# Optimization experiments

Hardware: AMD Instinct MI355X
Metric: run time of the kernel (lower is better)

The kernel has to match this reference:

```python
import jax, jax.numpy as jnp
import numpy as np

H = 32          # query heads
D = 128         # head_dim
THETA = 10000.0
NEG = -1e30


def _rope_cos_sin(positions, d):
    half = d // 2
    inv_freq = 1.0 / (THETA ** (jnp.arange(0, d, 2, dtype=jnp.float32) / d))  # [half]
    ang = positions.astype(jnp.float32)[:, None] * inv_freq[None, :]          # [B, half]
    return jnp.cos(ang), jnp.sin(ang)


def _apply_rope(x, cos, sin):
    # neox-style rotary on last dim; cos/sin broadcast over leading dims
    half = x.shape[-1] // 2
    x1, x2 = x[..., :half], x[..., half:]
    return jnp.concatenate([x1 * cos - x2 * sin, x2 * cos + x1 * sin], axis=-1)


def setup_inputs() -> dict:
    key = jax.random.key(0)
    ks = jax.random.split(key, 8)
    B, hidden = 64, 4096
    num_blocks, block_size, max_blocks = 16384, 16, 256
    hidden_states = jax.random.normal(ks[0], (B, hidden), dtype=jnp.float32)
    wqkv = jax.random.normal(ks[1], (hidden, (H + 2) * D), dtype=jnp.float32) * 0.02
    wdense = jax.random.normal(ks[2], (hidden, hidden), dtype=jnp.float32) * 0.02
    k_cache = jax.random.normal(ks[3], (num_blocks, block_size, D), dtype=jnp.float32)
    v_cache = jax.random.normal(ks[4], (num_blocks, block_size, D), dtype=jnp.float32)
    # each sequence owns a distinct set of 256 blocks
    block_tables = jnp.arange(B * max_blocks, dtype=jnp.int64).reshape(B, max_blocks)
    context_lens = jax.random.randint(ks[5], (B,), 1, max_blocks * block_size + 1).astype(jnp.int64)
    positions = context_lens - 1  # position of the new (current) token
    return {
        "hidden_states": hidden_states, "wqkv": wqkv, "wdense": wdense,
        "k_cache": k_cache, "v_cache": v_cache,
        "positions": positions, "block_tables": block_tables,
        "context_lens": context_lens,
    }


def reference(hidden_states, wqkv, wdense, k_cache, v_cache,
              positions, block_tables, context_lens):
    B = hidden_states.shape[0]
    block_size = k_cache.shape[1]
    scale = 1.0 / np.sqrt(D).astype(np.float32)

    # fused QKV projection (bias=False in Falcon-7B config)
    qkv = hidden_states @ wqkv                                  # [B,(H+2)*D]
    q = qkv[:, : H * D].reshape(B, H, D)
    k = qkv[:, H * D : (H + 1) * D]                             # [B,D]  (MQA, 1 kv head)
    v = qkv[:, (H + 1) * D :]                                   # [B,D]

    # rotary embedding on q and k at the current positions
    cos, sin = _rope_cos_sin(positions, D)                      # [B,D/2]
    q = _apply_rope(q, cos[:, None, :], sin[:, None, :])
    k = _apply_rope(k, cos, sin)

    # write the new token's k/v into the paged cache (scatter)
    rows = jnp.arange(B)
    blk = block_tables[rows, positions // block_size]           # [B]
    off = positions % block_size
    k_cache = k_cache.at[blk, off].set(k)
    v_cache = v_cache.at[blk, off].set(v)

    # paged gather: assemble each sequence's KV from its block table
    keys = k_cache[block_tables].reshape(B, -1, D)              # [B,L,D]
    vals = v_cache[block_tables].reshape(B, -1, D)
    L = keys.shape[1]

    scores = jnp.einsum('bhd,bld->bhl', q, keys) * scale        # [B,H,L]
    valid = jnp.arange(L)[None, :] < context_lens[:, None]      # [B,L]
    scores = jnp.where(valid[:, None, :], scores, NEG)
    probs = jax.nn.softmax(scores, axis=-1)
    attn = jnp.einsum('bhl,bld->bhd', probs, vals).reshape(B, H * D)

    return attn @ wdense                                        # [B,hidden]
```

## Files before the change

### kernel.cpp

```cpp
#include <hip/hip_runtime.h>
#include <hip/hip_bf16.h>
#include <cmath>

#define NHEADS 32
#define DIM 128
#define SPLITS 16
#define TILE 32
#define KSPLIT 16
#define QKV_N 4352
#define HID 4096

typedef __attribute__((ext_vector_type(4))) float f32x4;
typedef __attribute__((ext_vector_type(8))) short short8i;
typedef __attribute__((ext_vector_type(4))) short short4i;

__device__ __forceinline__ unsigned short f2bf(float x) {
  unsigned int b = __float_as_uint(x);
  return (unsigned short)((b + 0x7FFFu + ((b >> 16) & 1u)) >> 16);
}
__device__ __forceinline__ unsigned int pk2bf(float lo, float hi) {
  return (unsigned)f2bf(lo) | ((unsigned)f2bf(hi) << 16);
}

__device__ __forceinline__ f32x4 mfma16bf16(short4i a, short4i b, f32x4 c) {
#if __has_builtin(__builtin_amdgcn_mfma_f32_16x16x16bf16_1k)
  return __builtin_amdgcn_mfma_f32_16x16x16bf16_1k(a, b, c, 0, 0, 0);
#else
  asm volatile("v_mfma_f32_16x16x16_bf16 %0, %1, %2, %0"
               : "+v"(c) : "v"(a), "v"(b));
  return c;
#endif
}

__global__ __launch_bounds__(256, 4) void gemm64_mfma(
    const float* __restrict__ A, const float* __restrict__ W,
    float* __restrict__ P, int N, int K)
{
  __shared__ unsigned short Ab[64][40];
  __shared__ unsigned short Wt[64][40];
  const int t = threadIdx.x;
  const int w = t >> 6, lane = t & 63;
  const int l4 = lane >> 4, l16 = lane & 15;
  const int n0 = blockIdx.x * 64;
  const int KS = K / KSPLIT;
  const int kbase = blockIdx.y * KS;

  const int ar = t >> 2, akq = t & 3;
  const int bn = t & 63, bkq = t >> 6;

  f32x4 acc[4];
#pragma unroll
  for (int i = 0; i < 4; ++i) acc[i] = (f32x4){0.f, 0.f, 0.f, 0.f};

  float4 a0, a1;
  float bw[8];

#define GLOAD(KC)                                                          \
  {                                                                        \
    const float* ap = A + (size_t)ar * K + kbase + (KC) + akq * 8;         \
    a0 = *(const float4*)ap;                                               \
    a1 = *(const float4*)(ap + 4);                                         \
    const float* wp = W + (size_t)(kbase + (KC) + bkq * 8) * N + n0 + bn;  \
    _Pragma("unroll")                                                      \
    for (int j = 0; j < 8; ++j) bw[j] = wp[(size_t)j * N];                 \
  }

#define SWRITE                                                             \
  {                                                                        \
    unsigned int ua[4] = {pk2bf(a0.x, a0.y), pk2bf(a0.z, a0.w),            \
                          pk2bf(a1.x, a1.y), pk2bf(a1.z, a1.w)};           \
    *(float4*)&Ab[ar][akq * 8] = *(float4*)ua;                             \
    unsigned int ub[4] = {pk2bf(bw[0], bw[1]), pk2bf(bw[2], bw[3]),        \
                          pk2bf(bw[4], bw[5]), pk2bf(bw[6], bw[7])};       \
    *(float4*)&Wt[bn][bkq * 8] = *(float4*)ub;                             \
  }

  GLOAD(0);
  SWRITE;
  __syncthreads();

  for (int kc = 0; kc < KS; kc += 32) {
    const bool pre = (kc + 32 < KS);
    if (pre) GLOAD(kc + 32);

    const short8i af = *(const short8i*)&Ab[w * 16 + l16][l4 * 8];
#pragma unroll
    for (int nt = 0; nt < 4; ++nt) {
      const short8i bf = *(const short8i*)&Wt[nt * 16 + l16][l4 * 8];
      acc[nt] = __builtin_amdgcn_mfma_f32_16x16x32_bf16(af, bf, acc[nt], 0, 0, 0);
    }

    __syncthreads();
    if (pre) {
      SWRITE;
      __syncthreads();
    }
  }

  float* base = P + (size_t)blockIdx.y * 64 * N + n0;
#pragma unroll
  for (int nt = 0; nt < 4; ++nt)
#pragma unroll
    for (int r = 0; r < 4; ++r)
      base[(size_t)(w * 16 + l4 * 4 + r) * N + nt * 16 + l16] = acc[nt][r];
#undef GLOAD
#undef SWRITE
}

__global__ __launch_bounds__(256) void reduce_parts(
    const float* __restrict__ P, float* __restrict__ C, int total)
{
  const int i = (blockIdx.x * 256 + threadIdx.x) * 4;
  if (i >= total) return;
  float4 s = *(const float4*)(P + i);
#pragma unroll
  for (int k = 1; k < KSPLIT; ++k) {
    const float4 v = *(const float4*)(P + (size_t)k * total + i);
    s.x += v.x; s.y += v.y; s.z += v.z; s.w += v.w;
  }
  *(float4*)(C + i) = s;
}

__global__ __launch_bounds__(256) void rope_kernel(
    float* __restrict__ qkv, const int* __restrict__ positions)
{
  const int b = blockIdx.x;
  float* row = qkv + (size_t)b * QKV_N;
  const float pos = (float)positions[b];
  for (int it = threadIdx.x; it < 33 * 64; it += 256) {
    const int r = it >> 6, i = it & 63;
    float* x = row + (r < 32 ? r * DIM : HID);
    const float ex = (float)(2 * i) * (1.0f / 128.0f);
    const float inv = 1.0f / powf(10000.0f, ex);
    const float ang = pos * inv;
    const float c = cosf(ang), sn = sinf(ang);
    const float x1 = x[i], x2 = x[i + 64];
    x[i]      = x1 * c - x2 * sn;
    x[i + 64] = x2 * c + x1 * sn;
  }
}

__global__ __launch_bounds__(256, 4) void attn_kernel(
    const float* __restrict__ qkv,
    const float* __restrict__ k_cache, const float* __restrict__ v_cache,
    const int* __restrict__ block_tables, const int* __restrict__ context_lens,
    float* __restrict__ pm, float* __restrict__ pl, float* __restrict__ pacc)
{
  const int b = blockIdx.x, s = blockIdx.y;
  const int t = threadIdx.x;
  const int w = t >> 6, lane = t & 63;
  const int hq = w >> 1, pq = w & 1;
  const int l4 = lane >> 4, l16 = lane & 15;
  const int ctx = context_lens[b];
  const int pos = ctx - 1;
  const int chunk = (ctx + SPLITS - 1) / SPLITS;
  const int start = s * chunk;
  const int end = min(start + chunk, ctx);
  const int nt = (end > start) ? ((end - start + TILE - 1) / TILE) : 0;

  __shared__ unsigned short KbU[32 * 128];
  __shared__ unsigned short VtU[128 * 34];
  __shared__ float red[2][64][36];
  __shared__ int bt_lds[24];

  const float* qbase = qkv + (size_t)b * QKV_N;
  const int bt0 = start >> 4;
  if (t < 24) {
    const int idx = bt0 + t;
    bt_lds[t] = (idx < 256) ? block_tables[b * 256 + idx] : 0;
  }

  const float scale = 0.08838834764831845f;
  short8i qf[4];
  {
    const float* qp0 = qbase + (hq * 16 + l16) * DIM + l4 * 8;
#pragma unroll
    for (int ks = 0; ks < 4; ++ks) {
      const float4 a = *(const float4*)(qp0 + ks * 32);
      const float4 c = *(const float4*)(qp0 + ks * 32 + 4);
      short8i q;
      q[0] = (short)f2bf(a.x * scale); q[1] = (short)f2bf(a.y * scale);
      q[2] = (short)f2bf(a.z * scale); q[3] = (short)f2bf(a.w * scale);
      q[4] = (short)f2bf(c.x * scale); q[5] = (short)f2bf(c.y * scale);
      q[6] = (short)f2bf(c.z * scale); q[7] = (short)f2bf(c.w * scale);
      qf[ks] = q;
    }
  }

  f32x4 o2[8];
#pragma unroll
  for (int i = 0; i < 8; ++i) o2[i] = (f32x4){0.f, 0.f, 0.f, 0.f};
  float lh = 0.f;

  float4 kreg[4], vreg[4];
  const int tk_sub = t >> 5;
  const int tk_col = t & 31;

#define LOADREGS(T0)                                                     \
  {                                                                      \
    _Pragma("unroll")                                                    \
    for (int j = 0; j < 4; ++j) {                                        \
      int gp_ = (T0) + j * 8 + tk_sub;                                   \
      if (gp_ > pos) gp_ = pos;                                          \
      const float* kp;                                                   \
      if (gp_ == pos) kp = qbase + HID;                                  \
      else {                                                             \
        const int blk = bt_lds[(gp_ >> 4) - bt0];                        \
        kp = k_cache + ((size_t)blk * 16 + (gp_ & 15)) * DIM;            \
      }                                                                  \
      kreg[j] = *(const float4*)(kp + tk_col * 4);                       \
    }                                                                    \
    int gv = (T0) + tk_col;                                              \
    if (gv > pos) gv = pos;                                              \
    const float* vp;                                                     \
    if (gv == pos) vp = qbase + HID + DIM;                               \
    else {                                                               \
      const int blk = bt_lds[(gv >> 4) - bt0];                           \
      vp = v_cache + ((size_t)blk * 16 + (gv & 15)) * DIM;               \
    }                                                                    \
    _Pragma("unroll")                                                    \
    for (int j = 0; j < 4; ++j)                                          \
      vreg[j] = *(const float4*)(vp + tk_sub * 16 + j * 4);              \
  }

#define WRITE_TILE                                                                     \
  {                                                                                    \
    _Pragma("unroll")                                                                  \
    for (int j = 0; j < 4; ++j) {                                                      \
      const int pl_ = j * 8 + tk_sub;                                                  \
      const int up = (tk_col >> 1) ^ (pl_ & 15);                                       \
      unsigned int lo = pk2bf(kreg[j].x, kreg[j].y);                                   \
      unsigned int hi = pk2bf(kreg[j].z, kreg[j].w);                                   \
      unsigned int* dst = (unsigned int*)&KbU[pl_ * 128 + up * 8 + (tk_col & 1) * 4];  \
      dst[0] = lo; dst[1] = hi;                                                        \
    }                                                                                  \
    _Pragma("unroll")                                                                  \
    for (int j = 0; j < 4; ++j) {                                                      \
      const int od0 = tk_sub * 16 + j * 4;                                             \
      VtU[(od0 + 0) * 34 + tk_col] = f2bf(vreg[j].x);                                  \
      VtU[(od0 + 1) * 34 + tk_col] = f2bf(vreg[j].y);                                  \
      VtU[(od0 + 2) * 34 + tk_col] = f2bf(vreg[j].z);                                  \
      VtU[(od0 + 3) * 34 + tk_col] = f2bf(vreg[j].w);                                  \
    }                                                                                  \
  }

  if (nt > 0) {
    __syncthreads();
    LOADREGS(start);
    WRITE_TILE;
    __syncthreads();

    for (int it = 0; it < nt; ++it) {
      const int t0 = start + it * TILE;
      const bool pre = (it + 1 < nt);
      if (pre) LOADREGS(t0 + TILE);

      f32x4 accs = {0.f, 0.f, 0.f, 0.f};
      const int rowK = pq * 16 + l16;
#pragma unroll
      for (int ks = 0; ks < 4; ++ks) {
        const int up = (l4 + ks * 4) ^ l16;
        const short8i kf = *(const short8i*)&KbU[rowK * 128 + up * 8];
        accs = __builtin_amdgcn_mfma_f32_16x16x32_bf16(kf, qf[ks], accs, 0, 0, 0);
      }

      const int pb_ = t0 + pq * 16 + l4 * 4;
      const float p0 = (pb_ + 0 < end) ? __expf(accs[0]) : 0.f;
      const float p1 = (pb_ + 1 < end) ? __expf(accs[1]) : 0.f;
      const float p2 = (pb_ + 2 < end) ? __expf(accs[2]) : 0.f;
      const float p3 = (pb_ + 3 < end) ? __expf(accs[3]) : 0.f;
      lh += (p0 + p1) + (p2 + p3);
      union { unsigned int u[2]; short4i v; } pc;
      pc.u[0] = pk2bf(p0, p1);
      pc.u[1] = pk2bf(p2, p3);
      const short4i pf = pc.v;

      const int vb = pq * 16 + l4 * 4;
#pragma unroll
      for (int ob = 0; ob < 8; ++ob) {
        const int rowV = ob * 16 + l16;
        union { unsigned int u[2]; short4i v; } vc;
        vc.u[0] = *(const unsigned int*)&VtU[rowV * 34 + vb];
        vc.u[1] = *(const unsigned int*)&VtU[rowV * 34 + vb + 2];
        o2[ob] = mfma16bf16(pf, vc.v, o2[ob]);
      }

      if (pre) {
        __syncthreads();
        WRITE_TILE;
        __syncthreads();
      }
    }
  }

  float lhr = lh;
  lhr += __shfl_xor(lhr, 16);
  lhr += __shfl_xor(lhr, 32);

  if (pq == 1) {
#pragma unroll
    for (int ob = 0; ob < 8; ++ob) *(f32x4*)&red[hq][lane][ob * 4] = o2[ob];
    red[hq][lane][32] = lhr;
  }
  __syncthreads();
  if (pq == 0) {
#pragma unroll
    for (int ob = 0; ob < 8; ++ob) {
      const f32x4 r4 = *(const f32x4*)&red[hq][lane][ob * 4];
      o2[ob] += r4;
    }
    lhr += red[hq][lane][32];
    const size_t sbase = (size_t)(b * SPLITS + s) * NHEADS + hq * 16;
#pragma unroll
    for (int ob = 0; ob < 8; ++ob) {
      pacc[(sbase + l4 * 4 + 0) * DIM + ob * 16 + l16] = o2[ob][0];
      pacc[(sbase + l4 * 4 + 1) * DIM + ob * 16 + l16] = o2[ob][1];
      pacc[(sbase + l4 * 4 + 2) * DIM + ob * 16 + l16] = o2[ob][2];
      pacc[(sbase + l4 * 4 + 3) * DIM + ob * 16 + l16] = o2[ob][3];
    }
    if (lane < 16) { pm[sbase + lane] = 0.f; pl[sbase + lane] = lhr; }
  }
#undef LOADREGS
#undef WRITE_TILE
}

__global__ __launch_bounds__(128) void combine_kernel(
    const float* __restrict__ pm, const float* __restrict__ pl,
    const float* __restrict__ pacc, float* __restrict__ attn)
{
  const int bh = blockIdx.x;
  const int b = bh >> 5, h = bh & 31;
  const int d = threadIdx.x;
  float ms[SPLITS], ls[SPLITS];
  float M = -1e30f;
#pragma unroll
  for (int s = 0; s < SPLITS; ++s) {
    ms[s] = pm[(size_t)(b * SPLITS + s) * NHEADS + h];
    ls[s] = pl[(size_t)(b * SPLITS + s) * NHEADS + h];
    M = fmaxf(M, ms[s]);
  }
  float L = 0.f, o = 0.f;
#pragma unroll
  for (int s = 0; s < SPLITS; ++s) {
    const float wgt = __expf(ms[s] - M);
    L += ls[s] * wgt;
    o += wgt * pacc[((size_t)(b * SPLITS + s) * NHEADS + h) * DIM + d];
  }
  attn[(size_t)b * HID + h * DIM + d] = o / L;
}

extern "C" void kernel_launch(void* const* d_in, const int* in_sizes, int n_in,
                              void* d_out, int out_size, void* d_ws, size_t ws_size,
                              hipStream_t stream) {
  const float* hidden   = (const float*)d_in[0];
  const float* wqkv     = (const float*)d_in[1];
  const float* wdense   = (const float*)d_in[2];
  const float* k_cache  = (const float*)d_in[3];
  const float* v_cache  = (const float*)d_in[4];
  const int* positions    = (const int*)d_in[5];
  const int* block_tables = (const int*)d_in[6];
  const int* context_lens = (const int*)d_in[7];
  float* out = (float*)d_out;

  float* qkv  = (float*)d_ws;
  float* attn = qkv + 64 * QKV_N;
  float* un   = attn + 64 * HID;
  float* gp   = un;
  float* pacc = un;
  float* pm   = pacc + (size_t)64 * SPLITS * NHEADS * DIM;
  float* pl   = pm + 64 * SPLITS * NHEADS;

  gemm64_mfma<<<dim3(QKV_N / 64, KSPLIT), 256, 0, stream>>>(hidden, wqkv, gp, QKV_N, HID);
  reduce_parts<<<(64 * QKV_N) / 1024, 256, 0, stream>>>(gp, qkv, 64 * QKV_N);
  rope_kernel<<<64, 256, 0, stream>>>(qkv, positions);
  attn_kernel<<<dim3(64, SPLITS), 256, 0, stream>>>(qkv, k_cache, v_cache,
                                                    block_tables, context_lens, pm, pl, pacc);
  combine_kernel<<<64 * NHEADS, 128, 0, stream>>>(pm, pl, pacc, attn);
  gemm64_mfma<<<dim3(HID / 64, KSPLIT), 256, 0, stream>>>(attn, wdense, gp, HID, HID);
  reduce_parts<<<(64 * HID) / 1024, 256, 0, stream>>>(gp, out, 64 * HID);
}
```

Before: 103.8 us.

## Fuse split-K reduce with RoPE, halve K-splits, drop unused max buffer

Merges the QKV split-K reduction and the rotary embedding into one kernel, so the qkv tensor is no longer written and then re-read by a separate RoPE pass. It also halves the split-K factor for both GEMMs, which means fewer partial buffers to write and reduce but fewer blocks in each GEMM grid. It removes the per-split max array (always zero) from the attention and combine kernels, and switches bf16 conversion to the library intrinsic with packed stores. The mix of a tuning change and fusion means the GEMM occupancy tradeoff could go either way.

```diff
diff --git a/kernel.cpp b/kernel.cpp
--- a/kernel.cpp
+++ b/kernel.cpp
@@ -6,7 +6,7 @@
 #define DIM 128
 #define SPLITS 16
 #define TILE 32
-#define KSPLIT 16
+#define KSPLIT 8
 #define QKV_N 4352
 #define HID 4096
 
@@ -15,8 +15,8 @@
 typedef __attribute__((ext_vector_type(4))) short short4i;
 
 __device__ __forceinline__ unsigned short f2bf(float x) {
-  unsigned int b = __float_as_uint(x);
-  return (unsigned short)((b + 0x7FFFu + ((b >> 16) & 1u)) >> 16);
+  __hip_bfloat16 h = __float2bfloat16(x);
+  return *reinterpret_cast<unsigned short*>(&h);
 }
 __device__ __forceinline__ unsigned int pk2bf(float lo, float hi) {
   return (unsigned)f2bf(lo) | ((unsigned)f2bf(hi) << 16);
@@ -121,22 +121,56 @@
   *(float4*)(C + i) = s;
 }
 
-__global__ __launch_bounds__(256) void rope_kernel(
-    float* __restrict__ qkv, const int* __restrict__ positions)
+__global__ __launch_bounds__(256) void reduce_rope(
+    const float* __restrict__ P, float* __restrict__ qkv,
+    const int* __restrict__ positions)
 {
-  const int b = blockIdx.x;
-  float* row = qkv + (size_t)b * QKV_N;
-  const float pos = (float)positions[b];
-  for (int it = threadIdx.x; it < 33 * 64; it += 256) {
-    const int r = it >> 6, i = it & 63;
-    float* x = row + (r < 32 ? r * DIM : HID);
-    const float ex = (float)(2 * i) * (1.0f / 128.0f);
-    const float inv = 1.0f / powf(10000.0f, ex);
-    const float ang = pos * inv;
-    const float c = cosf(ang), sn = sinf(ang);
-    const float x1 = x[i], x2 = x[i + 64];
-    x[i]      = x1 * c - x2 * sn;
-    x[i + 64] = x2 * c + x1 * sn;
+  const int id = blockIdx.x * 256 + threadIdx.x;
+  const int b = id / 560;
+  const int w = id - b * 560;
+  const int total = 64 * QKV_N;
+  const size_t rbase = (size_t)b * QKV_N;
+
+  if (w < 528) {
+    const int r = w >> 4;
+    const int g = w & 15;
+    const int base = (r < 32) ? r * DIM : HID;
+    const int c1 = base + g * 4;
+    const int c2 = c1 + 64;
+    float4 s1 = *(const float4*)(P + rbase + c1);
+    float4 s2 = *(const float4*)(P + rbase + c2);
+#pragma unroll
+    for (int k = 1; k < KSPLIT; ++k) {
+      const float4 v1 = *(const float4*)(P + (size_t)k * total + rbase + c1);
+      const float4 v2 = *(const float4*)(P + (size_t)k * total + rbase + c2);
+      s1.x += v1.x; s1.y += v1.y; s1.z += v1.z; s1.w += v1.w;
+      s2.x += v2.x; s2.y += v2.y; s2.z += v2.z; s2.w += v2.w;
+    }
+    const float pos = (float)positions[b];
+    float o1[4], o2[4];
+    const float sv1[4] = {s1.x, s1.y, s1.z, s1.w};
+    const float sv2[4] = {s2.x, s2.y, s2.z, s2.w};
+#pragma unroll
+    for (int j = 0; j < 4; ++j) {
+      const int d = g * 4 + j;
+      const float ex = (float)d * (1.0f / 64.0f);
+      const float inv = 1.0f / powf(10000.0f, ex);
+      const float ang = pos * inv;
+      const float c = cosf(ang), sn = sinf(ang);
+      o1[j] = sv1[j] * c - sv2[j] * sn;
+      o2[j] = sv2[j] * c + sv1[j] * sn;
+    }
+    *(float4*)(qkv + rbase + c1) = make_float4(o1[0], o1[1], o1[2], o1[3]);
+    *(float4*)(qkv + rbase + c2) = make_float4(o2[0], o2[1], o2[2], o2[3]);
+  } else {
+    const int c = HID + DIM + (w - 528) * 4;
+    float4 s = *(const float4*)(P + rbase + c);
+#pragma unroll
+    for (int k = 1; k < KSPLIT; ++k) {
+      const float4 v = *(const float4*)(P + (size_t)k * total + rbase + c);
+      s.x += v.x; s.y += v.y; s.z += v.z; s.w += v.w;
+    }
+    *(float4*)(qkv + rbase + c) = s;
   }
 }
 
@@ -144,7 +178,7 @@
     const float* __restrict__ qkv,
     const float* __restrict__ k_cache, const float* __restrict__ v_cache,
     const int* __restrict__ block_tables, const int* __restrict__ context_lens,
-    float* __restrict__ pm, float* __restrict__ pl, float* __restrict__ pacc)
+    float* __restrict__ pl, float* __restrict__ pacc)
 {
   const int b = blockIdx.x, s = blockIdx.y;
   const int t = threadIdx.x;
@@ -178,12 +212,12 @@
     for (int ks = 0; ks < 4; ++ks) {
       const float4 a = *(const float4*)(qp0 + ks * 32);
       const float4 c = *(const float4*)(qp0 + ks * 32 + 4);
-      short8i q;
-      q[0] = (short)f2bf(a.x * scale); q[1] = (short)f2bf(a.y * scale);
-      q[2] = (short)f2bf(a.z * scale); q[3] = (short)f2bf(a.w * scale);
-      q[4] = (short)f2bf(c.x * scale); q[5] = (short)f2bf(c.y * scale);
-      q[6] = (short)f2bf(c.z * scale); q[7] = (short)f2bf(c.w * scale);
-      qf[ks] = q;
+      union { unsigned int u[4]; short8i v; } qc;
+      qc.u[0] = pk2bf(a.x * scale, a.y * scale);
+      qc.u[1] = pk2bf(a.z * scale, a.w * scale);
+      qc.u[2] = pk2bf(c.x * scale, c.y * scale);
+      qc.u[3] = pk2bf(c.z * scale, c.w * scale);
+      qf[ks] = qc.v;
     }
   }
 
@@ -318,33 +352,25 @@
       pacc[(sbase + l4 * 4 + 2) * DIM + ob * 16 + l16] = o2[ob][2];
       pacc[(sbase + l4 * 4 + 3) * DIM + ob * 16 + l16] = o2[ob][3];
     }
-    if (lane < 16) { pm[sbase + lane] = 0.f; pl[sbase + lane] = lhr; }
+    if (lane < 16) pl[sbase + lane] = lhr;
   }
 #undef LOADREGS
 #undef WRITE_TILE
 }
 
 __global__ __launch_bounds__(128) void combine_kernel(
-    const float* __restrict__ pm, const float* __restrict__ pl,
-    const float* __restrict__ pacc, float* __restrict__ attn)
+    const float* __restrict__ pl, const float* __restrict__ pacc,
+    float* __restrict__ attn)
 {
   const int bh = blockIdx.x;
   const int b = bh >> 5, h = bh & 31;
   const int d = threadIdx.x;
-  float ms[SPLITS], ls[SPLITS];
-  float M = -1e30f;
+  float L = 0.f, o = 0.f;
 #pragma unroll
   for (int s = 0; s < SPLITS; ++s) {
-    ms[s] = pm[(size_t)(b * SPLITS + s) * NHEADS + h];
-    ls[s] = pl[(size_t)(b * SPLITS + s) * NHEADS + h];
-    M = fmaxf(M, ms[s]);
-  }
-  float L = 0.f, o = 0.f;
-#pragma unroll
-  for (int s = 0; s < SPLITS; ++s) {
-    const float wgt = __expf(ms[s] - M);
-    L += ls[s] * wgt;
-    o += wgt * pacc[((size_t)(b * SPLITS + s) * NHEADS + h) * DIM + d];
+    const size_t idx = (size_t)(b * SPLITS + s) * NHEADS + h;
+    L += pl[idx];
+    o += pacc[idx * DIM + d];
   }
   attn[(size_t)b * HID + h * DIM + d] = o / L;
 }
@@ -367,15 +393,13 @@
   float* un   = attn + 64 * HID;
   float* gp   = un;
   float* pacc = un;
-  float* pm   = pacc + (size_t)64 * SPLITS * NHEADS * DIM;
-  float* pl   = pm + 64 * SPLITS * NHEADS;
+  float* pl   = pacc + (size_t)64 * SPLITS * NHEADS * DIM;
 
   gemm64_mfma<<<dim3(QKV_N / 64, KSPLIT), 256, 0, stream>>>(hidden, wqkv, gp, QKV_N, HID);
-  reduce_parts<<<(64 * QKV_N) / 1024, 256, 0, stream>>>(gp, qkv, 64 * QKV_N);
-  rope_kernel<<<64, 256, 0, stream>>>(qkv, positions);
+  reduce_rope<<<140, 256, 0, stream>>>(gp, qkv, positions);
   attn_kernel<<<dim3(64, SPLITS), 256, 0, stream>>>(qkv, k_cache, v_cache,
-                                                    block_tables, context_lens, pm, pl, pacc);
-  combine_kernel<<<64 * NHEADS, 128, 0, stream>>>(pm, pl, pacc, attn);
+                                                    block_tables, context_lens, pl, pacc);
+  combine_kernel<<<64 * NHEADS, 128, 0, stream>>>(pl, pacc, attn);
   gemm64_mfma<<<dim3(HID / 64, KSPLIT), 256, 0, stream>>>(attn, wdense, gp, HID, HID);
   reduce_parts<<<(64 * HID) / 1024, 256, 0, stream>>>(gp, out, 64 * HID);
 }
```

Measured after the change: 96.26 us. 7.3% less time.
